# Kernel tuning notes

Measured on AMD Instinct MI355X. Metric: run time of the kernel, lower is better.

The kernel has to match this reference:

```python
import jax, jax.numpy as jnp
import numpy as np

NUM_HEADS = 4
GROUPS = 8
EPS = 1e-5


def group_norm(x, w, b):
    B, C, H, W = x.shape
    xg = x.reshape(B, GROUPS, C // GROUPS, H, W)
    mu = jnp.mean(xg, axis=(2, 3, 4), keepdims=True)
    var = jnp.var(xg, axis=(2, 3, 4), keepdims=True)
    xg = (xg - mu) * jax.lax.rsqrt(var + EPS)
    x = xg.reshape(B, C, H, W)
    return x * w[None, :, None, None] + b[None, :, None, None]


def setup_inputs() -> dict:
    key = jax.random.key(0)
    k1, k2, k3 = jax.random.split(key, 3)
    B, C, H, W = 16, 256, 32, 32
    x = jax.random.normal(k1, (B, C, H, W), dtype=jnp.float32)
    gn_w = jnp.ones((C,), dtype=jnp.float32)
    gn_b = jnp.zeros((C,), dtype=jnp.float32)
    qkv_w = jax.random.normal(k2, (3 * C, C), dtype=jnp.float32) * 0.02
    qkv_b = jnp.zeros((3 * C,), dtype=jnp.float32)
    proj_w = jax.random.normal(k3, (C, C), dtype=jnp.float32) * 0.02
    proj_b = jnp.zeros((C,), dtype=jnp.float32)
    return {"x": x, "gn_w": gn_w, "gn_b": gn_b, "qkv_w": qkv_w,
            "qkv_b": qkv_b, "proj_w": proj_w, "proj_b": proj_b}


def reference(x, gn_w, gn_b, qkv_w, qkv_b, proj_w, proj_b):
    B, C, H, W = x.shape
    Dh = C // NUM_HEADS
    N = H * W
    skip = x
    xn = group_norm(x, gn_w, gn_b)
    # 1x1 conv QKV projection: [B,3C,H,W]
    qkv = jnp.einsum('oc,bchw->bohw', qkv_w, xn) + qkv_b[None, :, None, None]
    # split channel dim 3C -> [3, heads, Dh], flatten spatial -> N
    qkv = qkv.reshape(B, 3, NUM_HEADS, Dh, N)
    qkv = jnp.transpose(qkv, (1, 0, 2, 4, 3))  # [3,B,heads,N,Dh]
    q, k, v = qkv[0], qkv[1], qkv[2]
    scale = 1.0 / np.sqrt(Dh).astype(np.float32)
    attn = jnp.einsum('bhnd,bhmd->bhnm', q, k) * scale  # [B,heads,N,N]
    attn = jax.nn.softmax(attn, axis=-1)
    out = jnp.einsum('bhnm,bhmd->bhnd', attn, v)  # [B,heads,N,Dh]
    out = jnp.transpose(out, (0, 1, 3, 2)).reshape(B, C, H, W)
    out = jnp.einsum('oc,bchw->bohw', proj_w, out) + proj_b[None, :, None, None]
    return out + skip
```

## Files before the change

kernel.cpp:

```cpp
#include <hip/hip_runtime.h>

typedef unsigned short u16;
typedef __bf16 bf16x8 __attribute__((ext_vector_type(8)));
typedef float f32x4 __attribute__((ext_vector_type(4)));

#define QSCALE 0.18033688011112042f

__device__ __forceinline__ u16 f2bf(float f) {
  __bf16 h = (__bf16)f;
  union { __bf16 b; u16 u; } cv;
  cv.b = h;
  return cv.u;
}
__device__ __forceinline__ unsigned pack2(float a, float b) {
  return (unsigned)f2bf(a) | ((unsigned)f2bf(b) << 16);
}

__global__ __launch_bounds__(256) void prep(
    const float* __restrict__ qw, const float* __restrict__ pw,
    const float* __restrict__ x,
    u16* __restrict__ qwb, u16* __restrict__ pwb, float* __restrict__ stats) {
  __shared__ float sh1[256], sh2[256];
  const int blk = blockIdx.x;
  const int t = threadIdx.x;
  if (blk < 256) {
    int i = blk * 256 + t;
    const float* s; u16* d; int j;
    if (i < 49152) { s = qw; d = qwb; j = i; }
    else           { s = pw; d = pwb; j = i - 49152; }
    float4 v = *(const float4*)(s + (size_t)j * 4);
    uint2 o; o.x = pack2(v.x, v.y); o.y = pack2(v.z, v.w);
    *(uint2*)(d + (size_t)j * 4) = o;
    return;
  }
  const int bid = blk - 256;
  int cl = t >> 3;
  int off = (t & 7) * 4;
  const float* p = x + (size_t)bid * 32768 + (size_t)cl * 1024 + off;
  float s = 0.f, ss = 0.f;
#pragma unroll 8
  for (int i = 0; i < 32; ++i) {
    float4 v = *(const float4*)(p + i * 32);
    s += v.x + v.y + v.z + v.w;
    ss += v.x * v.x + v.y * v.y + v.z * v.z + v.w * v.w;
  }
  sh1[t] = s; sh2[t] = ss;
  __syncthreads();
  for (int st = 128; st > 0; st >>= 1) {
    if (t < st) { sh1[t] += sh1[t + st]; sh2[t] += sh2[t + st]; }
    __syncthreads();
  }
  if (t == 0) {
    float mean = sh1[0] * (1.f / 32768.f);
    float var = sh2[0] * (1.f / 32768.f) - mean * mean;
    stats[bid * 2] = mean;
    stats[bid * 2 + 1] = rsqrtf(var + 1e-5f);
  }
}

__global__ __launch_bounds__(256) void gn_apply_t(
    const float* __restrict__ x, const float* __restrict__ stats,
    const float* __restrict__ gw, const float* __restrict__ gb,
    u16* __restrict__ xnt) {
  int bid = blockIdx.x;
  int b = bid >> 6, ct = (bid >> 4) & 3, nt = bid & 15;
  int c0 = ct * 64, n0 = nt * 64;
  int t = threadIdx.x;
  __shared__ float tile[64][65];
  {
    int cl = t >> 2, nc = (t & 3) * 16;
    int c = c0 + cl, g = c >> 5;
    float mu = stats[(b * 8 + g) * 2], rs = stats[(b * 8 + g) * 2 + 1];
    float w = gw[c] * rs, bb = gb[c] - mu * w;
    const float* p = x + ((size_t)(b * 256 + c)) * 1024 + n0 + nc;
#pragma unroll
    for (int i = 0; i < 16; i += 4) {
      float4 v = *(const float4*)(p + i);
      tile[cl][nc + i + 0] = v.x * w + bb;
      tile[cl][nc + i + 1] = v.y * w + bb;
      tile[cl][nc + i + 2] = v.z * w + bb;
      tile[cl][nc + i + 3] = v.w * w + bb;
    }
  }
  __syncthreads();
  int nl = t >> 2, cc = (t & 3) * 16;
  float v[16];
#pragma unroll
  for (int i = 0; i < 16; ++i) v[i] = tile[cc + i][nl];
  uint4 w0, w1;
  w0.x = pack2(v[0], v[1]);  w0.y = pack2(v[2], v[3]);
  w0.z = pack2(v[4], v[5]);  w0.w = pack2(v[6], v[7]);
  w1.x = pack2(v[8], v[9]);  w1.y = pack2(v[10], v[11]);
  w1.z = pack2(v[12], v[13]); w1.w = pack2(v[14], v[15]);
  u16* q = xnt + ((size_t)(b * 1024 + n0 + nl)) * 256 + c0 + cc;
  *(uint4*)q = w0;
  *(uint4*)(q + 8) = w1;
}

template <int EPI>
__global__ __launch_bounds__(256) void gemm_nt(
    const u16* __restrict__ A, const u16* __restrict__ Bm,
    const float* __restrict__ bias,
    u16* __restrict__ o_q, u16* __restrict__ o_k, u16* __restrict__ o_v,
    const float* __restrict__ skip, float* __restrict__ out) {
  const int m0 = blockIdx.y * 128;
  const int n0 = blockIdx.x * 128;
  const int t = threadIdx.x;
  const int wave = t >> 6, lane = t & 63, lm = lane & 15, quad = lane >> 4;
  const int wr = wave >> 1, wc = wave & 1;

  __shared__ u16 As[2][128 * 32];
  __shared__ u16 Bs[2][128 * 32];

  f32x4 acc[4][4];
  const f32x4 fzero = {0.f, 0.f, 0.f, 0.f};
#pragma unroll
  for (int i = 0; i < 4; ++i)
#pragma unroll
    for (int j = 0; j < 4; ++j) acc[i][j] = fzero;

  const int srow = t >> 2, scol = (t & 3) * 8;
  const u16* pA0 = A + (size_t)(m0 + srow) * 256 + scol;
  const u16* pA1 = A + (size_t)(m0 + 64 + srow) * 256 + scol;
  const u16* pB0 = Bm + (size_t)(n0 + srow) * 256 + scol;
  const u16* pB1 = Bm + (size_t)(n0 + 64 + srow) * 256 + scol;

  uint4 pa0 = *(const uint4*)pA0;
  uint4 pa1 = *(const uint4*)pA1;
  uint4 pb0 = *(const uint4*)pB0;
  uint4 pb1 = *(const uint4*)pB1;
  *(uint4*)(As[0] + srow * 32 + scol) = pa0;
  *(uint4*)(As[0] + (64 + srow) * 32 + scol) = pa1;
  *(uint4*)(Bs[0] + srow * 32 + scol) = pb0;
  *(uint4*)(Bs[0] + (64 + srow) * 32 + scol) = pb1;
  pa0 = *(const uint4*)(pA0 + 32);
  pa1 = *(const uint4*)(pA1 + 32);
  pb0 = *(const uint4*)(pB0 + 32);
  pb1 = *(const uint4*)(pB1 + 32);

  for (int ki = 0; ki < 8; ++ki) {
    __syncthreads();
    if (ki + 1 < 8) {
      u16* as = As[(ki + 1) & 1];
      u16* bs = Bs[(ki + 1) & 1];
      *(uint4*)(as + srow * 32 + scol) = pa0;
      *(uint4*)(as + (64 + srow) * 32 + scol) = pa1;
      *(uint4*)(bs + srow * 32 + scol) = pb0;
      *(uint4*)(bs + (64 + srow) * 32 + scol) = pb1;
    }
    if (ki + 2 < 8) {
      const int ko = (ki + 2) * 32;
      pa0 = *(const uint4*)(pA0 + ko);
      pa1 = *(const uint4*)(pA1 + ko);
      pb0 = *(const uint4*)(pB0 + ko);
      pb1 = *(const uint4*)(pB1 + ko);
    }
    const u16* as = As[ki & 1];
    const u16* bs = Bs[ki & 1];
    bf16x8 af[4], bf[4];
#pragma unroll
    for (int mb = 0; mb < 4; ++mb)
      af[mb] = *(const bf16x8*)(as + (wr * 64 + mb * 16 + lm) * 32 + quad * 8);
#pragma unroll
    for (int nb = 0; nb < 4; ++nb)
      bf[nb] = *(const bf16x8*)(bs + (wc * 64 + nb * 16 + lm) * 32 + quad * 8);
#pragma unroll
    for (int mb = 0; mb < 4; ++mb)
#pragma unroll
      for (int nb = 0; nb < 4; ++nb)
        acc[mb][nb] = __builtin_amdgcn_mfma_f32_16x16x32_bf16(af[mb], bf[nb],
                                                              acc[mb][nb], 0, 0, 0);
  }

#pragma unroll
  for (int mb = 0; mb < 4; ++mb) {
#pragma unroll
    for (int nb = 0; nb < 4; ++nb) {
      const int o = m0 + wr * 64 + mb * 16 + 4 * quad;
      const int ng = n0 + wc * 64 + nb * 16 + lm;
      const int b = ng >> 10, n = ng & 1023;
      if (EPI == 0) {
        const int kind = o >> 8;
        if (kind == 1) {
          ushort4 pk;
          pk.x = f2bf(acc[mb][nb][0] + bias[o]);
          pk.y = f2bf(acc[mb][nb][1] + bias[o + 1]);
          pk.z = f2bf(acc[mb][nb][2] + bias[o + 2]);
          pk.w = f2bf(acc[mb][nb][3] + bias[o + 3]);
          const int h = (o >> 6) & 3;
          *(ushort4*)(o_k + ((size_t)((b * 4 + h) * 1024 + n)) * 64 + (o & 63)) = pk;
        } else {
          u16* dst = (kind == 0) ? o_q : o_v;
          const float sc = (kind == 0) ? QSCALE : 1.f;
          const int oc = o & 255;
#pragma unroll
          for (int r = 0; r < 4; ++r)
            dst[((size_t)(b * 256 + oc + r)) * 1024 + n] =
                f2bf((acc[mb][nb][r] + bias[o + r]) * sc);
        }
      } else {
#pragma unroll
        for (int r = 0; r < 4; ++r) {
          const size_t oi = ((size_t)(b * 256 + o + r)) * 1024 + n;
          out[oi] = acc[mb][nb][r] + bias[o + r] + skip[oi];
        }
      }
    }
  }
}

__global__ __launch_bounds__(256) void attn_fused(
    const u16* __restrict__ qdn, const u16* __restrict__ knd,
    const u16* __restrict__ vdn, u16* __restrict__ att) {
  const int bid = blockIdx.x;
  const int xcd = bid & 7, idx = bid >> 3;
  const int bh = xcd * 8 + (idx & 7);
  const int qtile = idx >> 3;
  const int t = threadIdx.x;
  const int wave = t >> 6, lane = t & 63, lm = lane & 15, quad = lane >> 4;

  const u16* qb = qdn + (size_t)bh * 65536;
  const u16* kb = knd + (size_t)bh * 65536;
  const u16* vb = vdn + (size_t)bh * 65536;

  __shared__ u16 KV[2][2][64 * 64];
  __shared__ u16 QP[64 * 64];

  const int e1 = t + 256;
  const int r0 = t >> 3, c0_ = t & 7, r1 = e1 >> 3, c1_ = e1 & 7;
  const int lk0 = r0 * 64 + ((c0_ ^ (r0 & 7)) * 8);
  const int lk1 = r1 * 64 + ((c1_ ^ (r1 & 7)) * 8);
  const u16* kg0 = kb + r0 * 64 + c0_ * 8;
  const u16* kg1 = kb + r1 * 64 + c1_ * 8;
  const u16* vg0 = vb + r0 * 1024 + c0_ * 8;
  const u16* vg1 = vb + r1 * 1024 + c1_ * 8;

  uint4 pk0 = *(const uint4*)kg0;
  uint4 pk1 = *(const uint4*)kg1;
  uint4 pv0 = *(const uint4*)vg0;
  uint4 pv1 = *(const uint4*)vg1;

  {
    union { uint4 v; u16 s[8]; } tq0, tq1;
    const int d0 = t >> 3, ngq = t & 7;
    tq0.v = *(const uint4*)(qb + (size_t)d0 * 1024 + qtile * 64 + ngq * 8);
    tq1.v = *(const uint4*)(qb + (size_t)(32 + d0) * 1024 + qtile * 64 + ngq * 8);
    const int oa = d0 >> 3, ob = 4 + oa, dl = d0 & 7;
#pragma unroll
    for (int k = 0; k < 8; ++k) {
      const int row = ngq * 8 + k;
      QP[row * 64 + ((oa ^ k) * 8) + dl] = tq0.s[k];
      QP[row * 64 + ((ob ^ k) * 8) + dl] = tq1.s[k];
    }
  }

  *(uint4*)(KV[0][0] + lk0) = pk0;
  *(uint4*)(KV[0][0] + lk1) = pk1;
  *(uint4*)(KV[0][1] + lk0) = pv0;
  *(uint4*)(KV[0][1] + lk1) = pv1;
  pk0 = *(const uint4*)(kg0 + 4096);
  pk1 = *(const uint4*)(kg1 + 4096);
  pv0 = *(const uint4*)(vg0 + 64);
  pv1 = *(const uint4*)(vg1 + 64);
  __syncthreads();

  const int qrow = wave * 16 + lm;
  u16* Pw = QP + qrow * 64;
  const int swz0 = (quad ^ (lm & 7)) * 8;
  const int swz1 = ((4 + quad) ^ (lm & 7)) * 8;
  const bf16x8 qf0 = *(const bf16x8*)(Pw + swz0);
  const bf16x8 qf1 = *(const bf16x8*)(Pw + swz1);

  const f32x4 fzero = {0.f, 0.f, 0.f, 0.f};
  f32x4 oacc[4];
#pragma unroll
  for (int d = 0; d < 4; ++d) oacc[d] = fzero;
  float lp = 0.f;

  for (int jc = 0; jc < 16; ++jc) {
    if (jc) __syncthreads();
    if (jc + 1 < 16) {
      u16* kd = KV[(jc + 1) & 1][0];
      u16* vd = KV[(jc + 1) & 1][1];
      *(uint4*)(kd + lk0) = pk0;
      *(uint4*)(kd + lk1) = pk1;
      *(uint4*)(vd + lk0) = pv0;
      *(uint4*)(vd + lk1) = pv1;
    }
    if (jc + 2 < 16) {
      pk0 = *(const uint4*)(kg0 + (jc + 2) * 4096);
      pk1 = *(const uint4*)(kg1 + (jc + 2) * 4096);
      pv0 = *(const uint4*)(vg0 + (jc + 2) * 64);
      pv1 = *(const uint4*)(vg1 + (jc + 2) * 64);
    }
    const u16* Ks = KV[jc & 1][0];
    const u16* Vs = KV[jc & 1][1];

    f32x4 sacc[4];
#pragma unroll
    for (int jb = 0; jb < 4; ++jb) sacc[jb] = fzero;
#pragma unroll
    for (int jb = 0; jb < 4; ++jb) {
      const int row = (jb * 16 + lm) * 64;
      bf16x8 kf0 = *(const bf16x8*)(Ks + row + swz0);
      bf16x8 kf1 = *(const bf16x8*)(Ks + row + swz1);
      sacc[jb] = __builtin_amdgcn_mfma_f32_16x16x32_bf16(kf0, qf0, sacc[jb], 0, 0, 0);
      sacc[jb] = __builtin_amdgcn_mfma_f32_16x16x32_bf16(kf1, qf1, sacc[jb], 0, 0, 0);
    }
#pragma unroll
    for (int jb = 0; jb < 4; ++jb) {
      const float e0 = exp2f(sacc[jb][0]);
      const float e1_ = exp2f(sacc[jb][1]);
      const float e2 = exp2f(sacc[jb][2]);
      const float e3 = exp2f(sacc[jb][3]);
      lp += (e0 + e1_) + (e2 + e3);
      ushort4 pw4;
      pw4.x = f2bf(e0); pw4.y = f2bf(e1_); pw4.z = f2bf(e2); pw4.w = f2bf(e3);
      const int oct = 2 * jb + (quad >> 1);
      *(ushort4*)(Pw + ((oct ^ (lm & 7)) * 8) + 4 * (quad & 1)) = pw4;
    }
    bf16x8 pf0 = *(const bf16x8*)(Pw + swz0);
    bf16x8 pf1 = *(const bf16x8*)(Pw + swz1);
#pragma unroll
    for (int db = 0; db < 4; ++db) {
      const int row = (db * 16 + lm) * 64;
      bf16x8 vf0 = *(const bf16x8*)(Vs + row + swz0);
      bf16x8 vf1 = *(const bf16x8*)(Vs + row + swz1);
      oacc[db] = __builtin_amdgcn_mfma_f32_16x16x32_bf16(pf0, vf0, oacc[db], 0, 0, 0);
      oacc[db] = __builtin_amdgcn_mfma_f32_16x16x32_bf16(pf1, vf1, oacc[db], 0, 0, 0);
    }
  }

  float rs = lp;
  rs += __shfl_xor(rs, 16);
  rs += __shfl_xor(rs, 32);
  const int b = bh >> 2, h = bh & 3;
#pragma unroll
  for (int r = 0; r < 4; ++r) {
    const float inv = 1.f / __shfl(rs, 4 * quad + r);
    const int n = qtile * 64 + wave * 16 + 4 * quad + r;
#pragma unroll
    for (int db = 0; db < 4; ++db) {
      const int c = h * 64 + db * 16 + lm;
      att[((size_t)(b * 1024 + n)) * 256 + c] = f2bf(oacc[db][r] * inv);
    }
  }
}

extern "C" void kernel_launch(void* const* d_in, const int* in_sizes, int n_in,
                              void* d_out, int out_size, void* d_ws, size_t ws_size,
                              hipStream_t stream) {
  const float* x      = (const float*)d_in[0];
  const float* gn_w   = (const float*)d_in[1];
  const float* gn_b   = (const float*)d_in[2];
  const float* qkv_w  = (const float*)d_in[3];
  const float* qkv_b  = (const float*)d_in[4];
  const float* proj_w = (const float*)d_in[5];
  const float* proj_b = (const float*)d_in[6];
  float* out = (float*)d_out;

  char* ws = (char*)d_ws;
  float* stats = (float*)(ws + 0);
  u16* qwb = (u16*)(ws + 4096);
  u16* pwb = (u16*)(ws + 397312);
  u16* xnt = (u16*)(ws + 528384);
  u16* qdn = (u16*)(ws + 8916992);
  u16* knd = (u16*)(ws + 17305600);
  u16* vdn = (u16*)(ws + 25694208);
  u16* att = (u16*)(ws + 34082816);

  prep<<<384, 256, 0, stream>>>(qkv_w, proj_w, x, qwb, pwb, stats);
  gn_apply_t<<<1024, 256, 0, stream>>>(x, stats, gn_w, gn_b, xnt);
  gemm_nt<0><<<dim3(128, 6), 256, 0, stream>>>(qwb, xnt, qkv_b, qdn, knd, vdn,
                                               nullptr, nullptr);
  attn_fused<<<1024, 256, 0, stream>>>(qdn, knd, vdn, att);
  gemm_nt<1><<<dim3(128, 2), 256, 0, stream>>>(pwb, att, proj_b, nullptr, nullptr,
                                               nullptr, x, out);
}
```

Measured before the change: 144.3 us.

## Double attention query tile per block and split projection GEMM into smaller tiles

The attention kernel now handles 128 query rows per block (two 16-row sub-tiles per wave), so each K/V chunk loaded into shared memory is reused across twice as many queries and the grid halves to 512 blocks. The projection GEMM becomes its own kernel with 64-row M tiles, doubling its grid to 512 blocks to fill more compute units. The cost is more registers per attention thread, a larger shared-memory footprint, and fewer attention blocks to hide latency.

```diff
diff --git a/kernel.cpp b/kernel.cpp
--- a/kernel.cpp
+++ b/kernel.cpp
@@ -97,12 +97,10 @@
   *(uint4*)(q + 8) = w1;
 }
 
-template <int EPI>
-__global__ __launch_bounds__(256) void gemm_nt(
+__global__ __launch_bounds__(256) void gemm_qkv(
     const u16* __restrict__ A, const u16* __restrict__ Bm,
     const float* __restrict__ bias,
-    u16* __restrict__ o_q, u16* __restrict__ o_k, u16* __restrict__ o_v,
-    const float* __restrict__ skip, float* __restrict__ out) {
+    u16* __restrict__ o_q, u16* __restrict__ o_k, u16* __restrict__ o_v) {
   const int m0 = blockIdx.y * 128;
   const int n0 = blockIdx.x * 128;
   const int t = threadIdx.x;
@@ -179,31 +177,106 @@
       const int o = m0 + wr * 64 + mb * 16 + 4 * quad;
       const int ng = n0 + wc * 64 + nb * 16 + lm;
       const int b = ng >> 10, n = ng & 1023;
-      if (EPI == 0) {
-        const int kind = o >> 8;
-        if (kind == 1) {
-          ushort4 pk;
-          pk.x = f2bf(acc[mb][nb][0] + bias[o]);
-          pk.y = f2bf(acc[mb][nb][1] + bias[o + 1]);
-          pk.z = f2bf(acc[mb][nb][2] + bias[o + 2]);
-          pk.w = f2bf(acc[mb][nb][3] + bias[o + 3]);
-          const int h = (o >> 6) & 3;
-          *(ushort4*)(o_k + ((size_t)((b * 4 + h) * 1024 + n)) * 64 + (o & 63)) = pk;
-        } else {
-          u16* dst = (kind == 0) ? o_q : o_v;
-          const float sc = (kind == 0) ? QSCALE : 1.f;
-          const int oc = o & 255;
-#pragma unroll
-          for (int r = 0; r < 4; ++r)
-            dst[((size_t)(b * 256 + oc + r)) * 1024 + n] =
-                f2bf((acc[mb][nb][r] + bias[o + r]) * sc);
-        }
+      const int kind = o >> 8;
+      if (kind == 1) {
+        ushort4 pk;
+        pk.x = f2bf(acc[mb][nb][0] + bias[o]);
+        pk.y = f2bf(acc[mb][nb][1] + bias[o + 1]);
+        pk.z = f2bf(acc[mb][nb][2] + bias[o + 2]);
+        pk.w = f2bf(acc[mb][nb][3] + bias[o + 3]);
+        const int h = (o >> 6) & 3;
+        *(ushort4*)(o_k + ((size_t)((b * 4 + h) * 1024 + n)) * 64 + (o & 63)) = pk;
       } else {
-#pragma unroll
-        for (int r = 0; r < 4; ++r) {
-          const size_t oi = ((size_t)(b * 256 + o + r)) * 1024 + n;
-          out[oi] = acc[mb][nb][r] + bias[o + r] + skip[oi];
-        }
+        u16* dst = (kind == 0) ? o_q : o_v;
+        const float sc = (kind == 0) ? QSCALE : 1.f;
+        const int oc = o & 255;
+#pragma unroll
+        for (int r = 0; r < 4; ++r)
+          dst[((size_t)(b * 256 + oc + r)) * 1024 + n] =
+              f2bf((acc[mb][nb][r] + bias[o + r]) * sc);
+      }
+    }
+  }
+}
+
+__global__ __launch_bounds__(256) void gemm_proj(
+    const u16* __restrict__ A, const u16* __restrict__ Bm,
+    const float* __restrict__ bias,
+    const float* __restrict__ skip, float* __restrict__ out) {
+  const int m0 = blockIdx.y * 64;
+  const int n0 = blockIdx.x * 128;
+  const int t = threadIdx.x;
+  const int wave = t >> 6, lane = t & 63, lm = lane & 15, quad = lane >> 4;
+  const int wr = wave >> 1, wc = wave & 1;
+
+  __shared__ u16 As[2][64 * 32];
+  __shared__ u16 Bs[2][128 * 32];
+
+  f32x4 acc[2][4];
+  const f32x4 fzero = {0.f, 0.f, 0.f, 0.f};
+#pragma unroll
+  for (int i = 0; i < 2; ++i)
+#pragma unroll
+    for (int j = 0; j < 4; ++j) acc[i][j] = fzero;
+
+  const int srow = t >> 2, scol = (t & 3) * 8;
+  const u16* pA0 = A + (size_t)(m0 + srow) * 256 + scol;
+  const u16* pB0 = Bm + (size_t)(n0 + srow) * 256 + scol;
+  const u16* pB1 = Bm + (size_t)(n0 + 64 + srow) * 256 + scol;
+
+  uint4 pa0 = *(const uint4*)pA0;
+  uint4 pb0 = *(const uint4*)pB0;
+  uint4 pb1 = *(const uint4*)pB1;
+  *(uint4*)(As[0] + srow * 32 + scol) = pa0;
+  *(uint4*)(Bs[0] + srow * 32 + scol) = pb0;
+  *(uint4*)(Bs[0] + (64 + srow) * 32 + scol) = pb1;
+  pa0 = *(const uint4*)(pA0 + 32);
+  pb0 = *(const uint4*)(pB0 + 32);
+  pb1 = *(const uint4*)(pB1 + 32);
+
+  for (int ki = 0; ki < 8; ++ki) {
+    __syncthreads();
+    if (ki + 1 < 8) {
+      u16* as = As[(ki + 1) & 1];
+      u16* bs = Bs[(ki + 1) & 1];
+      *(uint4*)(as + srow * 32 + scol) = pa0;
+      *(uint4*)(bs + srow * 32 + scol) = pb0;
+      *(uint4*)(bs + (64 + srow) * 32 + scol) = pb1;
+    }
+    if (ki + 2 < 8) {
+      const int ko = (ki + 2) * 32;
+      pa0 = *(const uint4*)(pA0 + ko);
+      pb0 = *(const uint4*)(pB0 + ko);
+      pb1 = *(const uint4*)(pB1 + ko);
+    }
+    const u16* as = As[ki & 1];
+    const u16* bs = Bs[ki & 1];
+    bf16x8 af[2], bf[4];
+#pragma unroll
+    for (int mb = 0; mb < 2; ++mb)
+      af[mb] = *(const bf16x8*)(as + (wr * 32 + mb * 16 + lm) * 32 + quad * 8);
+#pragma unroll
+    for (int nb = 0; nb < 4; ++nb)
+      bf[nb] = *(const bf16x8*)(bs + (wc * 64 + nb * 16 + lm) * 32 + quad * 8);
+#pragma unroll
+    for (int mb = 0; mb < 2; ++mb)
+#pragma unroll
+      for (int nb = 0; nb < 4; ++nb)
+        acc[mb][nb] = __builtin_amdgcn_mfma_f32_16x16x32_bf16(af[mb], bf[nb],
+                                                              acc[mb][nb], 0, 0, 0);
+  }
+
+#pragma unroll
+  for (int mb = 0; mb < 2; ++mb) {
+#pragma unroll
+    for (int nb = 0; nb < 4; ++nb) {
+      const int o = m0 + wr * 32 + mb * 16 + 4 * quad;
+      const int ng = n0 + wc * 64 + nb * 16 + lm;
+      const int b = ng >> 10, n = ng & 1023;
+#pragma unroll
+      for (int r = 0; r < 4; ++r) {
+        const size_t oi = ((size_t)(b * 256 + o + r)) * 1024 + n;
+        out[oi] = acc[mb][nb][r] + bias[o + r] + skip[oi];
       }
     }
   }
@@ -213,9 +286,8 @@
     const u16* __restrict__ qdn, const u16* __restrict__ knd,
     const u16* __restrict__ vdn, u16* __restrict__ att) {
   const int bid = blockIdx.x;
-  const int xcd = bid & 7, idx = bid >> 3;
-  const int bh = xcd * 8 + (idx & 7);
-  const int qtile = idx >> 3;
+  const int bh = (bid & 7) * 8 + ((bid >> 3) & 7);
+  const int qtile = bid >> 6;
   const int t = threadIdx.x;
   const int wave = t >> 6, lane = t & 63, lm = lane & 15, quad = lane >> 4;
 
@@ -224,7 +296,7 @@
   const u16* vb = vdn + (size_t)bh * 65536;
 
   __shared__ u16 KV[2][2][64 * 64];
-  __shared__ u16 QP[64 * 64];
+  __shared__ u16 QP[128 * 64];
 
   const int e1 = t + 256;
   const int r0 = t >> 3, c0_ = t & 7, r1 = e1 >> 3, c1_ = e1 & 7;
@@ -241,16 +313,21 @@
   uint4 pv1 = *(const uint4*)vg1;
 
   {
-    union { uint4 v; u16 s[8]; } tq0, tq1;
-    const int d0 = t >> 3, ngq = t & 7;
-    tq0.v = *(const uint4*)(qb + (size_t)d0 * 1024 + qtile * 64 + ngq * 8);
-    tq1.v = *(const uint4*)(qb + (size_t)(32 + d0) * 1024 + qtile * 64 + ngq * 8);
+    const int d0 = t >> 3, ng = t & 7;
+    const u16* qsl = qb + qtile * 128;
     const int oa = d0 >> 3, ob = 4 + oa, dl = d0 & 7;
 #pragma unroll
-    for (int k = 0; k < 8; ++k) {
-      const int row = ngq * 8 + k;
-      QP[row * 64 + ((oa ^ k) * 8) + dl] = tq0.s[k];
-      QP[row * 64 + ((ob ^ k) * 8) + dl] = tq1.s[k];
+    for (int half = 0; half < 2; ++half) {
+      const int ngg = ng + half * 8;
+      union { uint4 v; u16 s[8]; } a, bq;
+      a.v  = *(const uint4*)(qsl + (size_t)d0 * 1024 + ngg * 8);
+      bq.v = *(const uint4*)(qsl + (size_t)(32 + d0) * 1024 + ngg * 8);
+#pragma unroll
+      for (int k = 0; k < 8; ++k) {
+        const int row = ngg * 8 + k;
+        QP[row * 64 + ((oa ^ k) * 8) + dl] = a.s[k];
+        QP[row * 64 + ((ob ^ k) * 8) + dl] = bq.s[k];
+      }
     }
   }
 
@@ -264,18 +341,26 @@
   pv1 = *(const uint4*)(vg1 + 64);
   __syncthreads();
 
-  const int qrow = wave * 16 + lm;
-  u16* Pw = QP + qrow * 64;
   const int swz0 = (quad ^ (lm & 7)) * 8;
   const int swz1 = ((4 + quad) ^ (lm & 7)) * 8;
-  const bf16x8 qf0 = *(const bf16x8*)(Pw + swz0);
-  const bf16x8 qf1 = *(const bf16x8*)(Pw + swz1);
+
+  bf16x8 qf[2][2];
+  u16* Prow[2];
+#pragma unroll
+  for (int ib = 0; ib < 2; ++ib) {
+    u16* rp = QP + (wave * 32 + ib * 16 + lm) * 64;
+    qf[ib][0] = *(const bf16x8*)(rp + swz0);
+    qf[ib][1] = *(const bf16x8*)(rp + swz1);
+    Prow[ib] = rp;
+  }
 
   const f32x4 fzero = {0.f, 0.f, 0.f, 0.f};
-  f32x4 oacc[4];
-#pragma unroll
-  for (int d = 0; d < 4; ++d) oacc[d] = fzero;
-  float lp = 0.f;
+  f32x4 oacc[2][4];
+#pragma unroll
+  for (int ib = 0; ib < 2; ++ib)
+#pragma unroll
+    for (int d = 0; d < 4; ++d) oacc[ib][d] = fzero;
+  float lp[2] = {0.f, 0.f};
 
   for (int jc = 0; jc < 16; ++jc) {
     if (jc) __syncthreads();
@@ -296,53 +381,70 @@
     const u16* Ks = KV[jc & 1][0];
     const u16* Vs = KV[jc & 1][1];
 
-    f32x4 sacc[4];
-#pragma unroll
-    for (int jb = 0; jb < 4; ++jb) sacc[jb] = fzero;
+    f32x4 sacc[2][4];
+#pragma unroll
+    for (int ib = 0; ib < 2; ++ib)
+#pragma unroll
+      for (int jb = 0; jb < 4; ++jb) sacc[ib][jb] = fzero;
 #pragma unroll
     for (int jb = 0; jb < 4; ++jb) {
       const int row = (jb * 16 + lm) * 64;
       bf16x8 kf0 = *(const bf16x8*)(Ks + row + swz0);
       bf16x8 kf1 = *(const bf16x8*)(Ks + row + swz1);
-      sacc[jb] = __builtin_amdgcn_mfma_f32_16x16x32_bf16(kf0, qf0, sacc[jb], 0, 0, 0);
-      sacc[jb] = __builtin_amdgcn_mfma_f32_16x16x32_bf16(kf1, qf1, sacc[jb], 0, 0, 0);
-    }
-#pragma unroll
-    for (int jb = 0; jb < 4; ++jb) {
-      const float e0 = exp2f(sacc[jb][0]);
-      const float e1_ = exp2f(sacc[jb][1]);
-      const float e2 = exp2f(sacc[jb][2]);
-      const float e3 = exp2f(sacc[jb][3]);
-      lp += (e0 + e1_) + (e2 + e3);
-      ushort4 pw4;
-      pw4.x = f2bf(e0); pw4.y = f2bf(e1_); pw4.z = f2bf(e2); pw4.w = f2bf(e3);
-      const int oct = 2 * jb + (quad >> 1);
-      *(ushort4*)(Pw + ((oct ^ (lm & 7)) * 8) + 4 * (quad & 1)) = pw4;
-    }
-    bf16x8 pf0 = *(const bf16x8*)(Pw + swz0);
-    bf16x8 pf1 = *(const bf16x8*)(Pw + swz1);
+      sacc[0][jb] = __builtin_amdgcn_mfma_f32_16x16x32_bf16(kf0, qf[0][0], sacc[0][jb], 0, 0, 0);
+      sacc[0][jb] = __builtin_amdgcn_mfma_f32_16x16x32_bf16(kf1, qf[0][1], sacc[0][jb], 0, 0, 0);
+      sacc[1][jb] = __builtin_amdgcn_mfma_f32_16x16x32_bf16(kf0, qf[1][0], sacc[1][jb], 0, 0, 0);
+      sacc[1][jb] = __builtin_amdgcn_mfma_f32_16x16x32_bf16(kf1, qf[1][1], sacc[1][jb], 0, 0, 0);
+    }
+#pragma unroll
+    for (int ib = 0; ib < 2; ++ib) {
+#pragma unroll
+      for (int jb = 0; jb < 4; ++jb) {
+        const float e0 = exp2f(sacc[ib][jb][0]);
+        const float ee1 = exp2f(sacc[ib][jb][1]);
+        const float e2 = exp2f(sacc[ib][jb][2]);
+        const float e3 = exp2f(sacc[ib][jb][3]);
+        lp[ib] += (e0 + ee1) + (e2 + e3);
+        uint2 pw;
+        pw.x = pack2(e0, ee1);
+        pw.y = pack2(e2, e3);
+        const int oct = 2 * jb + (quad >> 1);
+        *(uint2*)(Prow[ib] + ((oct ^ (lm & 7)) * 8) + 4 * (quad & 1)) = pw;
+      }
+    }
+    bf16x8 pf[2][2];
+#pragma unroll
+    for (int ib = 0; ib < 2; ++ib) {
+      pf[ib][0] = *(const bf16x8*)(Prow[ib] + swz0);
+      pf[ib][1] = *(const bf16x8*)(Prow[ib] + swz1);
+    }
 #pragma unroll
     for (int db = 0; db < 4; ++db) {
       const int row = (db * 16 + lm) * 64;
       bf16x8 vf0 = *(const bf16x8*)(Vs + row + swz0);
       bf16x8 vf1 = *(const bf16x8*)(Vs + row + swz1);
-      oacc[db] = __builtin_amdgcn_mfma_f32_16x16x32_bf16(pf0, vf0, oacc[db], 0, 0, 0);
-      oacc[db] = __builtin_amdgcn_mfma_f32_16x16x32_bf16(pf1, vf1, oacc[db], 0, 0, 0);
-    }
-  }
-
-  float rs = lp;
-  rs += __shfl_xor(rs, 16);
-  rs += __shfl_xor(rs, 32);
+      oacc[0][db] = __builtin_amdgcn_mfma_f32_16x16x32_bf16(pf[0][0], vf0, oacc[0][db], 0, 0, 0);
+      oacc[0][db] = __builtin_amdgcn_mfma_f32_16x16x32_bf16(pf[0][1], vf1, oacc[0][db], 0, 0, 0);
+      oacc[1][db] = __builtin_amdgcn_mfma_f32_16x16x32_bf16(pf[1][0], vf0, oacc[1][db], 0, 0, 0);
+      oacc[1][db] = __builtin_amdgcn_mfma_f32_16x16x32_bf16(pf[1][1], vf1, oacc[1][db], 0, 0, 0);
+    }
+  }
+
   const int b = bh >> 2, h = bh & 3;
 #pragma unroll
-  for (int r = 0; r < 4; ++r) {
-    const float inv = 1.f / __shfl(rs, 4 * quad + r);
-    const int n = qtile * 64 + wave * 16 + 4 * quad + r;
-#pragma unroll
-    for (int db = 0; db < 4; ++db) {
-      const int c = h * 64 + db * 16 + lm;
-      att[((size_t)(b * 1024 + n)) * 256 + c] = f2bf(oacc[db][r] * inv);
+  for (int ib = 0; ib < 2; ++ib) {
+    float rs = lp[ib];
+    rs += __shfl_xor(rs, 16);
+    rs += __shfl_xor(rs, 32);
+#pragma unroll
+    for (int r = 0; r < 4; ++r) {
+      const float inv = 1.f / __shfl(rs, 4 * quad + r);
+      const int n = qtile * 128 + wave * 32 + ib * 16 + 4 * quad + r;
+#pragma unroll
+      for (int db = 0; db < 4; ++db) {
+        const int c = h * 64 + db * 16 + lm;
+        att[((size_t)(b * 1024 + n)) * 256 + c] = f2bf(oacc[ib][db][r] * inv);
+      }
     }
   }
 }
@@ -371,9 +473,7 @@
 
   prep<<<384, 256, 0, stream>>>(qkv_w, proj_w, x, qwb, pwb, stats);
   gn_apply_t<<<1024, 256, 0, stream>>>(x, stats, gn_w, gn_b, xnt);
-  gemm_nt<0><<<dim3(128, 6), 256, 0, stream>>>(qwb, xnt, qkv_b, qdn, knd, vdn,
-                                               nullptr, nullptr);
-  attn_fused<<<1024, 256, 0, stream>>>(qdn, knd, vdn, att);
-  gemm_nt<1><<<dim3(128, 2), 256, 0, stream>>>(pwb, att, proj_b, nullptr, nullptr,
-                                               nullptr, x, out);
-}
+  gemm_qkv<<<dim3(128, 6), 256, 0, stream>>>(qwb, xnt, qkv_b, qdn, knd, vdn);
+  attn_fused<<<512, 256, 0, stream>>>(qdn, knd, vdn, att);
+  gemm_proj<<<dim3(128, 4), 256, 0, stream>>>(pwb, att, proj_b, x, out);
+}
```

Result: no change. 143.3 us (-0.7%).

## Fuse group-norm apply into QKV GEMM operand load and shrink projection tile

Applied to the files above, without the earlier changes.

Removes the separate gn_apply_t kernel and the bf16 transposed intermediate by loading x directly in the QKV GEMM, normalizing it, converting to bf16 and storing it into swizzled shared memory. Blocks are remapped so each XCD works on a contiguous batch slice. The projection GEMM now uses 64-row M tiles, which doubles its block count for better occupancy. Both GEMMs gain an extra barrier per k-step, and the fused loader reads strided fp32 columns, which trades one kernel launch and an HBM round-trip for more per-block work.

```diff
diff --git a/kernel.cpp b/kernel.cpp
--- a/kernel.cpp
+++ b/kernel.cpp
@@ -58,83 +58,183 @@
   }
 }
 
-__global__ __launch_bounds__(256) void gn_apply_t(
-    const float* __restrict__ x, const float* __restrict__ stats,
+__global__ __launch_bounds__(256) void gemm_qkv(
+    const u16* __restrict__ A, const float* __restrict__ x,
+    const float* __restrict__ stats,
     const float* __restrict__ gw, const float* __restrict__ gb,
-    u16* __restrict__ xnt) {
-  int bid = blockIdx.x;
-  int b = bid >> 6, ct = (bid >> 4) & 3, nt = bid & 15;
-  int c0 = ct * 64, n0 = nt * 64;
-  int t = threadIdx.x;
-  __shared__ float tile[64][65];
-  {
-    int cl = t >> 2, nc = (t & 3) * 16;
-    int c = c0 + cl, g = c >> 5;
-    float mu = stats[(b * 8 + g) * 2], rs = stats[(b * 8 + g) * 2 + 1];
-    float w = gw[c] * rs, bb = gb[c] - mu * w;
-    const float* p = x + ((size_t)(b * 256 + c)) * 1024 + n0 + nc;
-#pragma unroll
-    for (int i = 0; i < 16; i += 4) {
-      float4 v = *(const float4*)(p + i);
-      tile[cl][nc + i + 0] = v.x * w + bb;
-      tile[cl][nc + i + 1] = v.y * w + bb;
-      tile[cl][nc + i + 2] = v.z * w + bb;
-      tile[cl][nc + i + 3] = v.w * w + bb;
-    }
-  }
-  __syncthreads();
-  int nl = t >> 2, cc = (t & 3) * 16;
-  float v[16];
-#pragma unroll
-  for (int i = 0; i < 16; ++i) v[i] = tile[cc + i][nl];
-  uint4 w0, w1;
-  w0.x = pack2(v[0], v[1]);  w0.y = pack2(v[2], v[3]);
-  w0.z = pack2(v[4], v[5]);  w0.w = pack2(v[6], v[7]);
-  w1.x = pack2(v[8], v[9]);  w1.y = pack2(v[10], v[11]);
-  w1.z = pack2(v[12], v[13]); w1.w = pack2(v[14], v[15]);
-  u16* q = xnt + ((size_t)(b * 1024 + n0 + nl)) * 256 + c0 + cc;
-  *(uint4*)q = w0;
-  *(uint4*)(q + 8) = w1;
-}
-
-template <int EPI>
-__global__ __launch_bounds__(256) void gemm_nt(
+    const float* __restrict__ bias,
+    u16* __restrict__ o_q, u16* __restrict__ o_k, u16* __restrict__ o_v) {
+  const int l = blockIdx.x;
+  const int xcd = l & 7;
+  const int i2 = l >> 3;
+  const int m_t = i2 % 6;
+  const int nl6 = i2 / 6;
+  const int nt = xcd * 16 + nl6;
+  const int m0 = m_t * 128;
+  const int n0 = nt * 128;
+  const int b = nt >> 3;
+  const int nsp0 = (nt & 7) * 128;
+
+  const int t = threadIdx.x;
+  const int wave = t >> 6, lane = t & 63, lm = lane & 15, quad = lane >> 4;
+  const int wr = wave >> 1, wc = wave & 1;
+
+  __shared__ u16 As[2][128 * 32];
+  __shared__ u16 Bs[2][128 * 32];
+
+  f32x4 acc[4][4];
+  const f32x4 fzero = {0.f, 0.f, 0.f, 0.f};
+#pragma unroll
+  for (int i = 0; i < 4; ++i)
+#pragma unroll
+    for (int j = 0; j < 4; ++j) acc[i][j] = fzero;
+
+  const int srow = t >> 2, scol = (t & 3) * 8;
+  const u16* pA0 = A + (size_t)(m0 + srow) * 256 + scol;
+  const u16* pA1 = A + (size_t)(m0 + 64 + srow) * 256 + scol;
+
+  const int n2 = t & 63, gq = t >> 6;
+  const float* xb = x + (size_t)b * 262144 + nsp0 + 2 * n2;
+  const int gsw = (gq ^ (n2 & 3)) * 8;
+  u16* const bd0 = (u16*)0;
+  (void)bd0;
+
+  float2 vB[8];
+  uint4 vA0, vA1;
+
+#define LD_B(ki)                                                       \
+  {                                                                    \
+    const int cb = (ki) * 32 + gq * 8;                                 \
+    _Pragma("unroll") for (int i = 0; i < 8; ++i)                      \
+        vB[i] = *(const float2*)(xb + (size_t)(cb + i) * 1024);        \
+  }
+#define ST_B(ki, buf)                                                  \
+  {                                                                    \
+    const int cb = (ki) * 32 + gq * 8;                                 \
+    const float mu = stats[(b * 8 + (ki)) * 2];                        \
+    const float rq = stats[(b * 8 + (ki)) * 2 + 1];                    \
+    float e0[8], e1[8];                                                \
+    _Pragma("unroll") for (int i = 0; i < 8; ++i) {                    \
+      const float w = gw[cb + i] * rq;                                 \
+      const float bb = gb[cb + i] - mu * w;                            \
+      e0[i] = vB[i].x * w + bb;                                        \
+      e1[i] = vB[i].y * w + bb;                                        \
+    }                                                                  \
+    uint4 w0, w1;                                                      \
+    w0.x = pack2(e0[0], e0[1]); w0.y = pack2(e0[2], e0[3]);            \
+    w0.z = pack2(e0[4], e0[5]); w0.w = pack2(e0[6], e0[7]);            \
+    w1.x = pack2(e1[0], e1[1]); w1.y = pack2(e1[2], e1[3]);            \
+    w1.z = pack2(e1[4], e1[5]); w1.w = pack2(e1[6], e1[7]);            \
+    *(uint4*)(Bs[buf] + (2 * n2) * 32 + gsw) = w0;                     \
+    *(uint4*)(Bs[buf] + (2 * n2 + 1) * 32 + gsw) = w1;                 \
+  }
+
+  LD_B(0);
+  vA0 = *(const uint4*)pA0;
+  vA1 = *(const uint4*)pA1;
+  ST_B(0, 0);
+  *(uint4*)(As[0] + srow * 32 + scol) = vA0;
+  *(uint4*)(As[0] + (64 + srow) * 32 + scol) = vA1;
+  LD_B(1);
+  vA0 = *(const uint4*)(pA0 + 32);
+  vA1 = *(const uint4*)(pA1 + 32);
+
+  for (int ki = 0; ki < 8; ++ki) {
+    __syncthreads();
+    if (ki + 1 < 8) {
+      ST_B(ki + 1, (ki + 1) & 1);
+      u16* as = As[(ki + 1) & 1];
+      *(uint4*)(as + srow * 32 + scol) = vA0;
+      *(uint4*)(as + (64 + srow) * 32 + scol) = vA1;
+    }
+    if (ki + 2 < 8) {
+      LD_B(ki + 2);
+      vA0 = *(const uint4*)(pA0 + (ki + 2) * 32);
+      vA1 = *(const uint4*)(pA1 + (ki + 2) * 32);
+    }
+    if (ki + 1 < 8) __syncthreads();
+    const u16* as = As[ki & 1];
+    const u16* bs = Bs[ki & 1];
+    bf16x8 af[4], bf[4];
+#pragma unroll
+    for (int mb = 0; mb < 4; ++mb)
+      af[mb] = *(const bf16x8*)(as + (wr * 64 + mb * 16 + lm) * 32 + quad * 8);
+#pragma unroll
+    for (int nb = 0; nb < 4; ++nb) {
+      const int row = wc * 64 + nb * 16 + lm;
+      bf[nb] = *(const bf16x8*)(bs + row * 32 + ((quad ^ ((row >> 1) & 3)) * 8));
+    }
+#pragma unroll
+    for (int mb = 0; mb < 4; ++mb)
+#pragma unroll
+      for (int nb = 0; nb < 4; ++nb)
+        acc[mb][nb] = __builtin_amdgcn_mfma_f32_16x16x32_bf16(af[mb], bf[nb],
+                                                              acc[mb][nb], 0, 0, 0);
+  }
+#undef LD_B
+#undef ST_B
+
+#pragma unroll
+  for (int mb = 0; mb < 4; ++mb) {
+#pragma unroll
+    for (int nb = 0; nb < 4; ++nb) {
+      const int o = m0 + wr * 64 + mb * 16 + 4 * quad;
+      const int ng = n0 + wc * 64 + nb * 16 + lm;
+      const int bb = ng >> 10, n = ng & 1023;
+      const int kind = o >> 8;
+      if (kind == 1) {
+        ushort4 pk;
+        pk.x = f2bf(acc[mb][nb][0] + bias[o]);
+        pk.y = f2bf(acc[mb][nb][1] + bias[o + 1]);
+        pk.z = f2bf(acc[mb][nb][2] + bias[o + 2]);
+        pk.w = f2bf(acc[mb][nb][3] + bias[o + 3]);
+        const int h = (o >> 6) & 3;
+        *(ushort4*)(o_k + ((size_t)((bb * 4 + h) * 1024 + n)) * 64 + (o & 63)) = pk;
+      } else {
+        u16* dst = (kind == 0) ? o_q : o_v;
+        const float sc = (kind == 0) ? QSCALE : 1.f;
+        const int oc = o & 255;
+#pragma unroll
+        for (int r = 0; r < 4; ++r)
+          dst[((size_t)(bb * 256 + oc + r)) * 1024 + n] =
+              f2bf((acc[mb][nb][r] + bias[o + r]) * sc);
+      }
+    }
+  }
+}
+
+__global__ __launch_bounds__(256) void gemm_proj(
     const u16* __restrict__ A, const u16* __restrict__ Bm,
     const float* __restrict__ bias,
-    u16* __restrict__ o_q, u16* __restrict__ o_k, u16* __restrict__ o_v,
     const float* __restrict__ skip, float* __restrict__ out) {
-  const int m0 = blockIdx.y * 128;
+  const int m0 = blockIdx.y * 64;
   const int n0 = blockIdx.x * 128;
   const int t = threadIdx.x;
   const int wave = t >> 6, lane = t & 63, lm = lane & 15, quad = lane >> 4;
   const int wr = wave >> 1, wc = wave & 1;
 
-  __shared__ u16 As[2][128 * 32];
+  __shared__ u16 As[2][64 * 32];
   __shared__ u16 Bs[2][128 * 32];
 
-  f32x4 acc[4][4];
+  f32x4 acc[2][4];
   const f32x4 fzero = {0.f, 0.f, 0.f, 0.f};
 #pragma unroll
-  for (int i = 0; i < 4; ++i)
+  for (int i = 0; i < 2; ++i)
 #pragma unroll
     for (int j = 0; j < 4; ++j) acc[i][j] = fzero;
 
   const int srow = t >> 2, scol = (t & 3) * 8;
   const u16* pA0 = A + (size_t)(m0 + srow) * 256 + scol;
-  const u16* pA1 = A + (size_t)(m0 + 64 + srow) * 256 + scol;
   const u16* pB0 = Bm + (size_t)(n0 + srow) * 256 + scol;
   const u16* pB1 = Bm + (size_t)(n0 + 64 + srow) * 256 + scol;
 
   uint4 pa0 = *(const uint4*)pA0;
-  uint4 pa1 = *(const uint4*)pA1;
   uint4 pb0 = *(const uint4*)pB0;
   uint4 pb1 = *(const uint4*)pB1;
   *(uint4*)(As[0] + srow * 32 + scol) = pa0;
-  *(uint4*)(As[0] + (64 + srow) * 32 + scol) = pa1;
   *(uint4*)(Bs[0] + srow * 32 + scol) = pb0;
   *(uint4*)(Bs[0] + (64 + srow) * 32 + scol) = pb1;
   pa0 = *(const uint4*)(pA0 + 32);
-  pa1 = *(const uint4*)(pA1 + 32);
   pb0 = *(const uint4*)(pB0 + 32);
   pb1 = *(const uint4*)(pB1 + 32);
 
@@ -144,28 +244,27 @@
       u16* as = As[(ki + 1) & 1];
       u16* bs = Bs[(ki + 1) & 1];
       *(uint4*)(as + srow * 32 + scol) = pa0;
-      *(uint4*)(as + (64 + srow) * 32 + scol) = pa1;
       *(uint4*)(bs + srow * 32 + scol) = pb0;
       *(uint4*)(bs + (64 + srow) * 32 + scol) = pb1;
     }
     if (ki + 2 < 8) {
       const int ko = (ki + 2) * 32;
       pa0 = *(const uint4*)(pA0 + ko);
-      pa1 = *(const uint4*)(pA1 + ko);
       pb0 = *(const uint4*)(pB0 + ko);
       pb1 = *(const uint4*)(pB1 + ko);
     }
+    if (ki + 1 < 8) __syncthreads();
     const u16* as = As[ki & 1];
     const u16* bs = Bs[ki & 1];
-    bf16x8 af[4], bf[4];
-#pragma unroll
-    for (int mb = 0; mb < 4; ++mb)
-      af[mb] = *(const bf16x8*)(as + (wr * 64 + mb * 16 + lm) * 32 + quad * 8);
+    bf16x8 af[2], bf[4];
+#pragma unroll
+    for (int mb = 0; mb < 2; ++mb)
+      af[mb] = *(const bf16x8*)(as + (wr * 32 + mb * 16 + lm) * 32 + quad * 8);
 #pragma unroll
     for (int nb = 0; nb < 4; ++nb)
       bf[nb] = *(const bf16x8*)(bs + (wc * 64 + nb * 16 + lm) * 32 + quad * 8);
 #pragma unroll
-    for (int mb = 0; mb < 4; ++mb)
+    for (int mb = 0; mb < 2; ++mb)
 #pragma unroll
       for (int nb = 0; nb < 4; ++nb)
         acc[mb][nb] = __builtin_amdgcn_mfma_f32_16x16x32_bf16(af[mb], bf[nb],
@@ -173,37 +272,16 @@
   }
 
 #pragma unroll
-  for (int mb = 0; mb < 4; ++mb) {
+  for (int mb = 0; mb < 2; ++mb) {
 #pragma unroll
     for (int nb = 0; nb < 4; ++nb) {
-      const int o = m0 + wr * 64 + mb * 16 + 4 * quad;
+      const int o = m0 + wr * 32 + mb * 16 + 4 * quad;
       const int ng = n0 + wc * 64 + nb * 16 + lm;
       const int b = ng >> 10, n = ng & 1023;
-      if (EPI == 0) {
-        const int kind = o >> 8;
-        if (kind == 1) {
-          ushort4 pk;
-          pk.x = f2bf(acc[mb][nb][0] + bias[o]);
-          pk.y = f2bf(acc[mb][nb][1] + bias[o + 1]);
-          pk.z = f2bf(acc[mb][nb][2] + bias[o + 2]);
-          pk.w = f2bf(acc[mb][nb][3] + bias[o + 3]);
-          const int h = (o >> 6) & 3;
-          *(ushort4*)(o_k + ((size_t)((b * 4 + h) * 1024 + n)) * 64 + (o & 63)) = pk;
-        } else {
-          u16* dst = (kind == 0) ? o_q : o_v;
-          const float sc = (kind == 0) ? QSCALE : 1.f;
-          const int oc = o & 255;
-#pragma unroll
-          for (int r = 0; r < 4; ++r)
-            dst[((size_t)(b * 256 + oc + r)) * 1024 + n] =
-                f2bf((acc[mb][nb][r] + bias[o + r]) * sc);
-        }
-      } else {
-#pragma unroll
-        for (int r = 0; r < 4; ++r) {
-          const size_t oi = ((size_t)(b * 256 + o + r)) * 1024 + n;
-          out[oi] = acc[mb][nb][r] + bias[o + r] + skip[oi];
-        }
+#pragma unroll
+      for (int r = 0; r < 4; ++r) {
+        const size_t oi = ((size_t)(b * 256 + o + r)) * 1024 + n;
+        out[oi] = acc[mb][nb][r] + bias[o + r] + skip[oi];
       }
     }
   }
@@ -213,9 +291,8 @@
     const u16* __restrict__ qdn, const u16* __restrict__ knd,
     const u16* __restrict__ vdn, u16* __restrict__ att) {
   const int bid = blockIdx.x;
-  const int xcd = bid & 7, idx = bid >> 3;
-  const int bh = xcd * 8 + (idx & 7);
-  const int qtile = idx >> 3;
+  const int bh = (bid & 7) * 8 + ((bid >> 3) & 7);
+  const int qtile = bid >> 6;
   const int t = threadIdx.x;
   const int wave = t >> 6, lane = t & 63, lm = lane & 15, quad = lane >> 4;
 
@@ -264,10 +341,9 @@
   pv1 = *(const uint4*)(vg1 + 64);
   __syncthreads();
 
-  const int qrow = wave * 16 + lm;
-  u16* Pw = QP + qrow * 64;
   const int swz0 = (quad ^ (lm & 7)) * 8;
   const int swz1 = ((4 + quad) ^ (lm & 7)) * 8;
+  u16* Pw = QP + (wave * 16 + lm) * 64;
   const bf16x8 qf0 = *(const bf16x8*)(Pw + swz0);
   const bf16x8 qf1 = *(const bf16x8*)(Pw + swz1);
 
@@ -310,14 +386,15 @@
 #pragma unroll
     for (int jb = 0; jb < 4; ++jb) {
       const float e0 = exp2f(sacc[jb][0]);
-      const float e1_ = exp2f(sacc[jb][1]);
+      const float ee1 = exp2f(sacc[jb][1]);
       const float e2 = exp2f(sacc[jb][2]);
       const float e3 = exp2f(sacc[jb][3]);
-      lp += (e0 + e1_) + (e2 + e3);
-      ushort4 pw4;
-      pw4.x = f2bf(e0); pw4.y = f2bf(e1_); pw4.z = f2bf(e2); pw4.w = f2bf(e3);
+      lp += (e0 + ee1) + (e2 + e3);
+      uint2 pw;
+      pw.x = pack2(e0, ee1);
+      pw.y = pack2(e2, e3);
       const int oct = 2 * jb + (quad >> 1);
-      *(ushort4*)(Pw + ((oct ^ (lm & 7)) * 8) + 4 * (quad & 1)) = pw4;
+      *(uint2*)(Pw + ((oct ^ (lm & 7)) * 8) + 4 * (quad & 1)) = pw;
     }
     bf16x8 pf0 = *(const bf16x8*)(Pw + swz0);
     bf16x8 pf1 = *(const bf16x8*)(Pw + swz1);
@@ -363,17 +440,14 @@
   float* stats = (float*)(ws + 0);
   u16* qwb = (u16*)(ws + 4096);
   u16* pwb = (u16*)(ws + 397312);
-  u16* xnt = (u16*)(ws + 528384);
   u16* qdn = (u16*)(ws + 8916992);
   u16* knd = (u16*)(ws + 17305600);
   u16* vdn = (u16*)(ws + 25694208);
   u16* att = (u16*)(ws + 34082816);
 
   prep<<<384, 256, 0, stream>>>(qkv_w, proj_w, x, qwb, pwb, stats);
-  gn_apply_t<<<1024, 256, 0, stream>>>(x, stats, gn_w, gn_b, xnt);
-  gemm_nt<0><<<dim3(128, 6), 256, 0, stream>>>(qwb, xnt, qkv_b, qdn, knd, vdn,
-                                               nullptr, nullptr);
+  gemm_qkv<<<768, 256, 0, stream>>>(qwb, x, stats, gn_w, gn_b, qkv_b,
+                                    qdn, knd, vdn);
   attn_fused<<<1024, 256, 0, stream>>>(qdn, knd, vdn, att);
-  gemm_nt<1><<<dim3(128, 2), 256, 0, stream>>>(pwb, att, proj_b, nullptr, nullptr,
-                                               nullptr, x, out);
-}
+  gemm_proj<<<dim3(128, 4), 256, 0, stream>>>(pwb, att, proj_b, x, out);
+}
```

Result: no change. 142.9 us (-1.0%).
